# Performance work log

Measured on AMD Instinct MI355X. Metric: run time of the kernel, lower is better.

The kernel has to match this reference:

```python
import jax, jax.numpy as jnp
import numpy as np

B, N, IN_DIM, LATENT = 4, 4096, 1024, 128


def setup_inputs() -> dict:
    key = jax.random.key(0)
    ks = jax.random.split(key, 9)
    s_in = 1.0 / np.sqrt(IN_DIM)
    s_lat = 1.0 / np.sqrt(LATENT)
    return {
        "Q": jax.random.normal(ks[0], (B, N, IN_DIM), jnp.float32),
        "K": jax.random.normal(ks[1], (B, N, IN_DIM), jnp.float32),
        "V": jax.random.normal(ks[2], (B, N, IN_DIM), jnp.float32),
        "Wk": jax.random.uniform(ks[3], (LATENT, IN_DIM), jnp.float32, -s_in, s_in),
        "bk": jax.random.uniform(ks[4], (LATENT,), jnp.float32, -s_in, s_in),
        "Wq": jax.random.uniform(ks[5], (LATENT, LATENT), jnp.float32, -s_lat, s_lat),
        "bq": jax.random.uniform(ks[6], (LATENT,), jnp.float32, -s_lat, s_lat),
        "Wv": jax.random.uniform(ks[7], (LATENT, IN_DIM), jnp.float32, -s_in, s_in),
        "bv": jax.random.uniform(ks[8], (LATENT,), jnp.float32, -s_in, s_in),
    }


def reference(Q, K, V, Wk, bk, Wq, bq, Wv, bv):
    # NOTE: faithful to original quirks: input K is ignored; Q is re-projected
    # from key_prj(Q); qry_prj has in_dim == latent_dim for this to typecheck.
    Kp = jnp.einsum('bni,oi->bno', Q, Wk) + bk            # [B,N,LATENT]
    Qp = jnp.einsum('bnl,ol->bno', Kp, Wq) + bq           # [B,N,LATENT]
    Vp = jnp.einsum('bni,oi->bno', V, Wv) + bv            # [B,N,LATENT]
    n = Kp.shape[1]
    # score = bmm(K, Q^T) / sqrt(seq_len)  -> [B, N, N]
    scores = jnp.einsum('bnd,bmd->bnm', Kp, Qp) / jnp.sqrt(jnp.asarray(n, scores_dtype(Kp)))
    W = jax.nn.softmax(scores, axis=-2)                   # softmax over rows (dim=-2)
    # Y = (V^T @ W)^T = W^T @ V -> [B, N, LATENT]
    Y = jnp.einsum('bnm,bnd->bmd', W, Vp)
    return Y


def scores_dtype(x):
    return x.dtype
```

## Files before the change

kernel.cpp:

```cpp
#include <hip/hip_runtime.h>
#include <hip/hip_bf16.h>
#include <math.h>

#define NB     4
#define NTOK   4096
#define IND    1024
#define LAT    128
#define MTOT   (NB*NTOK)
#define L2E    1.4426950408889634f
#define SC2    0.022542110013890053f

typedef short bf16x8 __attribute__((ext_vector_type(8)));
typedef float f32x4  __attribute__((ext_vector_type(4)));
typedef float f32x16 __attribute__((ext_vector_type(16)));

__device__ __forceinline__ unsigned short f2bf(float x) {
    union { float f; unsigned int u; } v; v.f = x;
    unsigned int r = v.u + 0x7FFFu + ((v.u >> 16) & 1u);
    return (unsigned short)(r >> 16);
}
__device__ __forceinline__ float bf2f(unsigned short b) {
    union { unsigned int u; float f; } v; v.u = ((unsigned int)b) << 16;
    return v.f;
}
__device__ __forceinline__ unsigned cvtpk(float lo, float hi) {
    unsigned r;
    asm("v_cvt_pk_bf16_f32 %0, %1, %2" : "=v"(r) : "v"(lo), "v"(hi));
    return r;
}
__device__ __forceinline__ void permswap(unsigned &x, unsigned &y) {
    asm volatile("v_permlane32_swap_b32 %0, %1" : "+v"(x), "+v"(y));
}
__device__ __forceinline__ void gld16(const void* g, void* l) {
    __builtin_amdgcn_global_load_lds(
        (const __attribute__((address_space(1))) void*)g,
        (__attribute__((address_space(3))) void*)l, 16, 0, 0);
}

__global__ __launch_bounds__(256) void fuse_w(const float* __restrict__ Wq,
                                              const float* __restrict__ Wk,
                                              const float* __restrict__ bk,
                                              const float* __restrict__ bq,
                                              unsigned short* __restrict__ Wcomb,
                                              float* __restrict__ bqk) {
    const int o = blockIdx.y;
    const int i = blockIdx.x * 256 + threadIdx.x;
    Wcomb[(size_t)o * IND + i] = f2bf(Wk[(size_t)o * IND + i]);
    float acc = 0.f;
    #pragma unroll 8
    for (int l = 0; l < 128; ++l)
        acc = fmaf(Wq[o * 128 + l], Wk[(size_t)l * IND + i], acc);
    Wcomb[(size_t)(128 + o) * IND + i] = f2bf(acc * SC2);
    if (blockIdx.x == 0 && threadIdx.x == 0) {
        float b = bq[o];
        for (int l = 0; l < 128; ++l) b = fmaf(Wq[o * 128 + l], bk[l], b);
        bqk[o] = b * SC2;
    }
}

__global__ __launch_bounds__(256, 2) void proj_qk(const float* __restrict__ X,
                                                  const unsigned short* __restrict__ Wcomb,
                                                  const float* __restrict__ bk,
                                                  const float* __restrict__ bqk,
                                                  unsigned short* __restrict__ Kp,
                                                  unsigned short* __restrict__ Qp) {
    __shared__ __align__(16) char lds[4096 + 32768];
    const int t = threadIdx.x, l = t & 63, w = t >> 6;
    const int br = blockIdx.x;
    const int lrow = l & 15, lhi = l >> 4;
    const int wr = (w >> 1) * 16, wc = (w & 1) * 128;

    f32x4 acc[8] = {};

    float4 aR[2];
    bf16x8 bR[8];
    #pragma unroll
    for (int j = 0; j < 2; ++j) {
        int c = t + j * 256, row = c >> 4, ch = c & 15;
        aR[j] = *(const float4*)&X[(size_t)(br * 32 + row) * IND + ch * 4];
    }
    #pragma unroll
    for (int j = 0; j < 8; ++j) {
        int c = t + j * 256, row = c >> 3, ch = c & 7;
        bR[j] = *(const bf16x8*)&Wcomb[(size_t)row * IND + ch * 8];
    }

    for (int k0 = 0; k0 < IND; k0 += 64) {
        #pragma unroll
        for (int j = 0; j < 2; ++j) {
            int c = t + j * 256, row = c >> 4, ch = c & 15;
            union { unsigned short s[4]; unsigned long long q; } pk;
            pk.s[0] = f2bf(aR[j].x); pk.s[1] = f2bf(aR[j].y);
            pk.s[2] = f2bf(aR[j].z); pk.s[3] = f2bf(aR[j].w);
            *(unsigned long long*)(lds + ((row * 128 + ch * 8) ^ ((row & 7) << 4))) = pk.q;
        }
        #pragma unroll
        for (int j = 0; j < 8; ++j) {
            int c = t + j * 256, row = c >> 3, ch = c & 7;
            *(bf16x8*)(lds + 4096 + ((row * 128 + ch * 16) ^ ((row & 7) << 4))) = bR[j];
        }
        if (k0 + 64 < IND) {
            #pragma unroll
            for (int j = 0; j < 2; ++j) {
                int c = t + j * 256, row = c >> 4, ch = c & 15;
                aR[j] = *(const float4*)&X[(size_t)(br * 32 + row) * IND + k0 + 64 + ch * 4];
            }
            #pragma unroll
            for (int j = 0; j < 8; ++j) {
                int c = t + j * 256, row = c >> 3, ch = c & 7;
                bR[j] = *(const bf16x8*)&Wcomb[(size_t)row * IND + k0 + 64 + ch * 8];
            }
        }
        __syncthreads();

        const int arow = wr + lrow;
        bf16x8 a[2];
        #pragma unroll
        for (int kk = 0; kk < 2; ++kk)
            a[kk] = *(const bf16x8*)(lds + ((arow * 128 + kk * 64 + lhi * 16) ^ ((arow & 7) << 4)));
        #pragma unroll
        for (int n = 0; n < 8; ++n) {
            const int brow = wc + n * 16 + lrow;
            #pragma unroll
            for (int kk = 0; kk < 2; ++kk) {
                bf16x8 b = *(const bf16x8*)(lds + 4096 +
                    ((brow * 128 + kk * 64 + lhi * 16) ^ ((brow & 7) << 4)));
                acc[n] = __builtin_amdgcn_mfma_f32_16x16x32_bf16(a[kk], b, acc[n], 0, 0, 0);
            }
        }
        __syncthreads();
    }

    const int row0 = br * 32 + wr + lhi * 4;
    unsigned short* out = (wc == 0) ? Kp : Qp;
    const float* bias = (wc == 0) ? bk : bqk;
    #pragma unroll
    for (int n = 0; n < 8; ++n) {
        int col = n * 16 + lrow;
        float bv = bias[col];
        #pragma unroll
        for (int r = 0; r < 4; ++r)
            out[(size_t)(row0 + r) * LAT + col] = f2bf(acc[n][r] + bv);
    }
}

__global__ __launch_bounds__(256, 2) void proj_v(const float* __restrict__ X,
                                                 const float* __restrict__ Wv,
                                                 const float* __restrict__ bv,
                                                 unsigned short* __restrict__ VpT) {
    __shared__ __align__(16) char lds[4096 + 16384];
    const int t = threadIdx.x, l = t & 63, w = t >> 6;
    const int br = blockIdx.x;
    const int lrow = l & 15, lhi = l >> 4;
    const int wr = (w >> 1) * 16, wc = (w & 1) * 64;

    f32x4 acc[4] = {};

    float4 aR[2], bR[8];
    #pragma unroll
    for (int j = 0; j < 2; ++j) {
        int c = t + j * 256, row = c >> 4, ch = c & 15;
        aR[j] = *(const float4*)&X[(size_t)(br * 32 + row) * IND + ch * 4];
    }
    #pragma unroll
    for (int j = 0; j < 8; ++j) {
        int c = t + j * 256, row = c >> 4, ch = c & 15;
        bR[j] = *(const float4*)&Wv[(size_t)row * IND + ch * 4];
    }

    for (int k0 = 0; k0 < IND; k0 += 64) {
        #pragma unroll
        for (int j = 0; j < 2; ++j) {
            int c = t + j * 256, row = c >> 4, ch = c & 15;
            union { unsigned short s[4]; unsigned long long q; } pk;
            pk.s[0] = f2bf(aR[j].x); pk.s[1] = f2bf(aR[j].y);
            pk.s[2] = f2bf(aR[j].z); pk.s[3] = f2bf(aR[j].w);
            *(unsigned long long*)(lds + ((row * 128 + ch * 8) ^ ((row & 7) << 4))) = pk.q;
        }
        #pragma unroll
        for (int j = 0; j < 8; ++j) {
            int c = t + j * 256, row = c >> 4, ch = c & 15;
            union { unsigned short s[4]; unsigned long long q; } pk;
            pk.s[0] = f2bf(bR[j].x); pk.s[1] = f2bf(bR[j].y);
            pk.s[2] = f2bf(bR[j].z); pk.s[3] = f2bf(bR[j].w);
            *(unsigned long long*)(lds + 4096 + ((row * 128 + ch * 8) ^ ((row & 7) << 4))) = pk.q;
        }
        if (k0 + 64 < IND) {
            #pragma unroll
            for (int j = 0; j < 2; ++j) {
                int c = t + j * 256, row = c >> 4, ch = c & 15;
                aR[j] = *(const float4*)&X[(size_t)(br * 32 + row) * IND + k0 + 64 + ch * 4];
            }
            #pragma unroll
            for (int j = 0; j < 8; ++j) {
                int c = t + j * 256, row = c >> 4, ch = c & 15;
                bR[j] = *(const float4*)&Wv[(size_t)row * IND + k0 + 64 + ch * 4];
            }
        }
        __syncthreads();

        const int arow = wr + lrow;
        bf16x8 a[2];
        #pragma unroll
        for (int kk = 0; kk < 2; ++kk)
            a[kk] = *(const bf16x8*)(lds + ((arow * 128 + kk * 64 + lhi * 16) ^ ((arow & 7) << 4)));
        #pragma unroll
        for (int n = 0; n < 4; ++n) {
            const int brow = wc + n * 16 + lrow;
            #pragma unroll
            for (int kk = 0; kk < 2; ++kk) {
                bf16x8 b = *(const bf16x8*)(lds + 4096 +
                    ((brow * 128 + kk * 64 + lhi * 16) ^ ((brow & 7) << 4)));
                acc[n] = __builtin_amdgcn_mfma_f32_16x16x32_bf16(a[kk], b, acc[n], 0, 0, 0);
            }
        }
        __syncthreads();
    }

    const int row0 = br * 32 + wr + lhi * 4;
    const int batch = row0 >> 12, tok = row0 & 4095;
    #pragma unroll
    for (int n = 0; n < 4; ++n) {
        int col = wc + n * 16 + lrow;
        float bv_ = bv[col];
        union { unsigned short s[4]; unsigned long long q; } pk;
        #pragma unroll
        for (int r = 0; r < 4; ++r) pk.s[r] = f2bf(acc[n][r] + bv_);
        *(unsigned long long*)&VpT[(size_t)batch * (LAT * NTOK) + (size_t)col * NTOK + tok] = pk.q;
    }
}

template<int NSPLIT>
__global__ __launch_bounds__(256, 3) void attn4(const unsigned short* __restrict__ Qp,
                                                const unsigned short* __restrict__ Kp,
                                                const unsigned short* __restrict__ VpT,
                                                unsigned short* __restrict__ Opart,
                                                float* __restrict__ lsum,
                                                float* __restrict__ Y) {
    __shared__ __align__(16) char ldsK[2][8192];
    __shared__ __align__(16) char ldsV[2][8192];
    const int t = threadIdx.x, l = t & 63, w = t >> 6;
    const int lane31 = l & 31, hi = l >> 5;

    int qt, b, ck;
    if constexpr (NSPLIT > 1) {
        int x = blockIdx.x;
        int glo = x & 7, rest = x >> 3;
        qt = rest & 31;
        int g = glo + 8 * (rest >> 5);
        b = g / NSPLIT; ck = g % NSPLIT;
    } else {
        qt = blockIdx.x & 31; b = blockIdx.x >> 5; ck = 0;
    }
    const size_t base  = (size_t)b * ((size_t)NTOK * LAT);
    const size_t vbase = (size_t)b * ((size_t)LAT * NTOK);
    const int wq = qt * 128 + w * 32;
    const int k_base = ck * (NTOK / NSPLIT);
    const int kts = (NTOK / NSPLIT) / 32;

    const int kc_row = t >> 4, kc_ch = t & 15;
    const int vc_row = t >> 2, vc_ch = t & 3;

    bf16x8 qf[8];
    {
        const size_t qrow = base + (size_t)(wq + lane31) * LAT;
        #pragma unroll
        for (int ds = 0; ds < 8; ++ds)
            qf[ds] = *(const bf16x8*)&Qp[qrow + ds * 16 + hi * 8];
    }

    f32x16 OA[4] = {};
    float lrun = 0.f;

    auto STAGE = [&](int bi, int k_lo) {
        #pragma unroll
        for (int j = 0; j < 2; ++j) {
            int row = kc_row + j * 16;
            gld16(&Kp[base + (size_t)(k_lo + row) * LAT + (kc_ch ^ (row & 15)) * 8],
                  &ldsK[bi][j * 4096 + w * 1024]);
        }
        #pragma unroll
        for (int j = 0; j < 2; ++j) {
            int row = vc_row + j * 64;
            gld16(&VpT[vbase + (size_t)row * NTOK + k_lo + (vc_ch ^ ((row >> 1) & 3)) * 8],
                  &ldsV[bi][j * 4096 + w * 1024]);
        }
    };

    int buf = 0;
    STAGE(0, k_base);
    asm volatile("s_waitcnt vmcnt(0)" ::: "memory");
    __syncthreads();

    for (int kt = 0; kt < kts; ++kt) {
        if (kt + 1 < kts) STAGE(buf ^ 1, k_base + (kt + 1) * 32);
        const char* lK = ldsK[buf];
        const char* lV = ldsV[buf];

        f32x16 SA;
        {
            f32x16 s = {};
            const int kr = lane31;
            __builtin_amdgcn_s_setprio(1);
            #pragma unroll
            for (int ds = 0; ds < 8; ++ds) {
                bf16x8 kf = *(const bf16x8*)(lK +
                    ((kr * 256 + ds * 32 + hi * 16) ^ ((kr & 15) << 4)));
                s = __builtin_amdgcn_mfma_f32_32x32x16_bf16(kf, qf[ds], s, 0, 0, 0);
            }
            __builtin_amdgcn_s_setprio(0);
            SA = s;
        }

        float p[16];
        #pragma unroll
        for (int r = 0; r < 16; ++r) {
            p[r] = exp2f(SA[r]);
            lrun += p[r];
        }
        unsigned a0 = cvtpk(p[0], p[1]),  a1 = cvtpk(p[2], p[3]);
        unsigned a2 = cvtpk(p[4], p[5]),  a3 = cvtpk(p[6], p[7]);
        permswap(a0, a2); permswap(a1, a3);
        unsigned b0 = cvtpk(p[8], p[9]),   b1 = cvtpk(p[10], p[11]);
        unsigned b2 = cvtpk(p[12], p[13]), b3 = cvtpk(p[14], p[15]);
        permswap(b0, b2); permswap(b1, b3);
        union { unsigned u[4]; bf16x8 v; } f0 = {{a0, a1, a2, a3}};
        union { unsigned u[4]; bf16x8 v; } f1 = {{b0, b1, b2, b3}};

        __builtin_amdgcn_s_setprio(1);
        #pragma unroll
        for (int db = 0; db < 4; ++db) {
            const int d = db * 32 + lane31;
            const int vsw = ((d >> 1) & 3) << 4;
            bf16x8 vfA = *(const bf16x8*)(lV + ((d * 64 + hi * 16) ^ vsw));
            OA[db] = __builtin_amdgcn_mfma_f32_32x32x16_bf16(vfA, f0.v, OA[db], 0, 0, 0);
            bf16x8 vfB = *(const bf16x8*)(lV + ((d * 64 + 32 + hi * 16) ^ vsw));
            OA[db] = __builtin_amdgcn_mfma_f32_32x32x16_bf16(vfB, f1.v, OA[db], 0, 0, 0);
        }
        __builtin_amdgcn_s_setprio(0);

        asm volatile("s_waitcnt vmcnt(0)" ::: "memory");
        __syncthreads();
        buf ^= 1;
    }

    const float ltot = lrun + __shfl_xor(lrun, 32);

    if constexpr (NSPLIT == 1) {
        const float inv = 1.0f / ltot;
        float* dst = &Y[base + (size_t)(wq + lane31) * LAT];
        #pragma unroll
        for (int db = 0; db < 4; ++db)
            #pragma unroll
            for (int g = 0; g < 4; ++g) {
                f32x4 v;
                #pragma unroll
                for (int j = 0; j < 4; ++j) v[j] = OA[db][4 * g + j] * inv;
                *(f32x4*)&dst[db * 32 + 8 * g + 4 * hi] = v;
            }
    } else {
        const size_t prow = (size_t)ck * MTOT + (size_t)b * NTOK + wq + lane31;
        unsigned short* dst = &Opart[prow * LAT];
        #pragma unroll
        for (int db = 0; db < 4; ++db)
            #pragma unroll
            for (int g = 0; g < 4; ++g) {
                union { unsigned short s[4]; unsigned long long q; } pk;
                #pragma unroll
                for (int j = 0; j < 4; ++j) pk.s[j] = f2bf(OA[db][4 * g + j]);
                *(unsigned long long*)&dst[db * 32 + 8 * g + 4 * hi] = pk.q;
            }
        if (l < 32) lsum[prow] = ltot;
    }
}

template<int S>
__global__ __launch_bounds__(256) void merge3(const unsigned short* __restrict__ Opart,
                                              const float* __restrict__ lsum,
                                              float* __restrict__ Y) {
    const int idx = blockIdx.x * 256 + threadIdx.x;
    const int row = idx >> 4, cc = (idx & 15) * 8;
    float L = 0.f;
    #pragma unroll
    for (int c = 0; c < S; ++c) L += lsum[(size_t)c * MTOT + row];
    float acc[8] = {};
    #pragma unroll
    for (int c = 0; c < S; ++c) {
        bf16x8 v = *(const bf16x8*)&Opart[((size_t)c * MTOT + row) * LAT + cc];
        #pragma unroll
        for (int j = 0; j < 8; ++j)
            acc[j] += bf2f((unsigned short)v[j]);
    }
    const float inv = 1.f / L;
    f32x4 o0, o1;
    #pragma unroll
    for (int j = 0; j < 4; ++j) { o0[j] = acc[j] * inv; o1[j] = acc[4 + j] * inv; }
    *(f32x4*)&Y[(size_t)row * LAT + cc] = o0;
    *(f32x4*)&Y[(size_t)row * LAT + cc + 4] = o1;
}

extern "C" void kernel_launch(void* const* d_in, const int* in_sizes, int n_in,
                              void* d_out, int out_size, void* d_ws, size_t ws_size,
                              hipStream_t stream) {
    const float* Q  = (const float*)d_in[0];
    const float* V  = (const float*)d_in[2];
    const float* Wk = (const float*)d_in[3];
    const float* bk = (const float*)d_in[4];
    const float* Wq = (const float*)d_in[5];
    const float* bq = (const float*)d_in[6];
    const float* Wv = (const float*)d_in[7];
    const float* bv = (const float*)d_in[8];
    float* Y = (float*)d_out;

    char* ws = (char*)d_ws;
    unsigned short* Kp    = (unsigned short*)(ws);
    unsigned short* Qp    = (unsigned short*)(ws + (4 << 20));
    unsigned short* VpT   = (unsigned short*)(ws + (8 << 20));
    unsigned short* Wcomb = (unsigned short*)(ws + (12 << 20));
    float*          bqk   = (float*)         (ws + 13107200);
    float*          lsum  = (float*)         (ws + 13107712);
    unsigned short* Opart = (unsigned short*)(ws + 14680064);
    const size_t need8 = 14680064 + (size_t)8 * MTOT * LAT * 2;
    const size_t need4 = 14680064 + (size_t)4 * MTOT * LAT * 2;

    fuse_w<<<dim3(4, 128), 256, 0, stream>>>(Wq, Wk, bk, bq, Wcomb, bqk);
    proj_qk<<<dim3(512), 256, 0, stream>>>(Q, Wcomb, bk, bqk, Kp, Qp);
    proj_v<<<dim3(512), 256, 0, stream>>>(V, Wv, bv, VpT);

    if (ws_size >= need8) {
        attn4<8><<<dim3(32 * NB * 8), 256, 0, stream>>>(Qp, Kp, VpT, Opart, lsum, nullptr);
        merge3<8><<<dim3(MTOT * 16 / 256), 256, 0, stream>>>(Opart, lsum, Y);
    } else if (ws_size >= need4) {
        attn4<4><<<dim3(32 * NB * 4), 256, 0, stream>>>(Qp, Kp, VpT, Opart, lsum, nullptr);
        merge3<4><<<dim3(MTOT * 16 / 256), 256, 0, stream>>>(Opart, lsum, Y);
    } else {
        attn4<1><<<dim3(32 * NB), 256, 0, stream>>>(Qp, Kp, VpT, nullptr, nullptr, Y);
    }
}
```

Measured before the change: 116.2 us.

## Process two 32-query tiles per wave to reuse K/V LDS fragments

Each wave now handles 64 query rows (two 32-row sub-tiles) instead of 32. Every K and V fragment loaded from LDS feeds two MFMAs, which halves LDS reads and global K/V staging per query. Block count is halved and launch bounds drop to 2 blocks per CU, since register use roughly doubles with two sets of Q fragments and accumulators. The risks are lower occupancy and fewer blocks to fill the GPU (512 with NSPLIT=8).

```diff
diff --git a/kernel.cpp b/kernel.cpp
--- a/kernel.cpp
+++ b/kernel.cpp
@@ -231,7 +231,7 @@
 }
 
 template<int NSPLIT>
-__global__ __launch_bounds__(256, 3) void attn4(const unsigned short* __restrict__ Qp,
+__global__ __launch_bounds__(256, 2) void attn6(const unsigned short* __restrict__ Qp,
                                                 const unsigned short* __restrict__ Kp,
                                                 const unsigned short* __restrict__ VpT,
                                                 unsigned short* __restrict__ Opart,
@@ -246,31 +246,20 @@
     if constexpr (NSPLIT > 1) {
         int x = blockIdx.x;
         int glo = x & 7, rest = x >> 3;
-        qt = rest & 31;
-        int g = glo + 8 * (rest >> 5);
+        qt = rest & 15;
+        int g = glo + 8 * (rest >> 4);
         b = g / NSPLIT; ck = g % NSPLIT;
     } else {
-        qt = blockIdx.x & 31; b = blockIdx.x >> 5; ck = 0;
+        qt = blockIdx.x & 15; b = blockIdx.x >> 4; ck = 0;
     }
     const size_t base  = (size_t)b * ((size_t)NTOK * LAT);
     const size_t vbase = (size_t)b * ((size_t)LAT * NTOK);
-    const int wq = qt * 128 + w * 32;
+    const int wq = qt * 256 + w * 64;
     const int k_base = ck * (NTOK / NSPLIT);
     const int kts = (NTOK / NSPLIT) / 32;
 
     const int kc_row = t >> 4, kc_ch = t & 15;
     const int vc_row = t >> 2, vc_ch = t & 3;
-
-    bf16x8 qf[8];
-    {
-        const size_t qrow = base + (size_t)(wq + lane31) * LAT;
-        #pragma unroll
-        for (int ds = 0; ds < 8; ++ds)
-            qf[ds] = *(const bf16x8*)&Qp[qrow + ds * 16 + hi * 8];
-    }
-
-    f32x16 OA[4] = {};
-    float lrun = 0.f;
 
     auto STAGE = [&](int bi, int k_lo) {
         #pragma unroll
@@ -287,6 +276,20 @@
         }
     };
 
+    bf16x8 qf0[8], qf1[8];
+    {
+        const size_t qr0 = base + (size_t)(wq + lane31) * LAT;
+        const size_t qr1 = base + (size_t)(wq + 32 + lane31) * LAT;
+        #pragma unroll
+        for (int ds = 0; ds < 8; ++ds) {
+            qf0[ds] = *(const bf16x8*)&Qp[qr0 + ds * 16 + hi * 8];
+            qf1[ds] = *(const bf16x8*)&Qp[qr1 + ds * 16 + hi * 8];
+        }
+    }
+
+    f32x16 OA0[4] = {}, OA1[4] = {};
+    float lr0 = 0.f, lr1 = 0.f;
+
     int buf = 0;
     STAGE(0, k_base);
     asm volatile("s_waitcnt vmcnt(0)" ::: "memory");
@@ -297,35 +300,47 @@
         const char* lK = ldsK[buf];
         const char* lV = ldsV[buf];
 
-        f32x16 SA;
+        f32x16 SA0 = {}, SA1 = {};
         {
-            f32x16 s = {};
             const int kr = lane31;
+            const int ksw = (kr & 15) << 4;
             __builtin_amdgcn_s_setprio(1);
             #pragma unroll
             for (int ds = 0; ds < 8; ++ds) {
-                bf16x8 kf = *(const bf16x8*)(lK +
-                    ((kr * 256 + ds * 32 + hi * 16) ^ ((kr & 15) << 4)));
-                s = __builtin_amdgcn_mfma_f32_32x32x16_bf16(kf, qf[ds], s, 0, 0, 0);
+                bf16x8 kf = *(const bf16x8*)(lK + ((kr * 256 + ds * 32 + hi * 16) ^ ksw));
+                SA0 = __builtin_amdgcn_mfma_f32_32x32x16_bf16(kf, qf0[ds], SA0, 0, 0, 0);
+                SA1 = __builtin_amdgcn_mfma_f32_32x32x16_bf16(kf, qf1[ds], SA1, 0, 0, 0);
             }
             __builtin_amdgcn_s_setprio(0);
-            SA = s;
-        }
-
-        float p[16];
-        #pragma unroll
-        for (int r = 0; r < 16; ++r) {
-            p[r] = exp2f(SA[r]);
-            lrun += p[r];
-        }
-        unsigned a0 = cvtpk(p[0], p[1]),  a1 = cvtpk(p[2], p[3]);
-        unsigned a2 = cvtpk(p[4], p[5]),  a3 = cvtpk(p[6], p[7]);
-        permswap(a0, a2); permswap(a1, a3);
-        unsigned b0 = cvtpk(p[8], p[9]),   b1 = cvtpk(p[10], p[11]);
-        unsigned b2 = cvtpk(p[12], p[13]), b3 = cvtpk(p[14], p[15]);
-        permswap(b0, b2); permswap(b1, b3);
-        union { unsigned u[4]; bf16x8 v; } f0 = {{a0, a1, a2, a3}};
-        union { unsigned u[4]; bf16x8 v; } f1 = {{b0, b1, b2, b3}};
+        }
+
+        union { unsigned u[4]; bf16x8 v; } f00, f01, f10, f11;
+        {
+            float p[16];
+            #pragma unroll
+            for (int r = 0; r < 16; ++r) { p[r] = exp2f(SA0[r]); lr0 += p[r]; }
+            unsigned a0 = cvtpk(p[0], p[1]),  a1 = cvtpk(p[2], p[3]);
+            unsigned a2 = cvtpk(p[4], p[5]),  a3 = cvtpk(p[6], p[7]);
+            permswap(a0, a2); permswap(a1, a3);
+            unsigned b0 = cvtpk(p[8], p[9]),   b1 = cvtpk(p[10], p[11]);
+            unsigned b2 = cvtpk(p[12], p[13]), b3 = cvtpk(p[14], p[15]);
+            permswap(b0, b2); permswap(b1, b3);
+            f00.u[0]=a0; f00.u[1]=a1; f00.u[2]=a2; f00.u[3]=a3;
+            f01.u[0]=b0; f01.u[1]=b1; f01.u[2]=b2; f01.u[3]=b3;
+        }
+        {
+            float p[16];
+            #pragma unroll
+            for (int r = 0; r < 16; ++r) { p[r] = exp2f(SA1[r]); lr1 += p[r]; }
+            unsigned a0 = cvtpk(p[0], p[1]),  a1 = cvtpk(p[2], p[3]);
+            unsigned a2 = cvtpk(p[4], p[5]),  a3 = cvtpk(p[6], p[7]);
+            permswap(a0, a2); permswap(a1, a3);
+            unsigned b0 = cvtpk(p[8], p[9]),   b1 = cvtpk(p[10], p[11]);
+            unsigned b2 = cvtpk(p[12], p[13]), b3 = cvtpk(p[14], p[15]);
+            permswap(b0, b2); permswap(b1, b3);
+            f10.u[0]=a0; f10.u[1]=a1; f10.u[2]=a2; f10.u[3]=a3;
+            f11.u[0]=b0; f11.u[1]=b1; f11.u[2]=b2; f11.u[3]=b3;
+        }
 
         __builtin_amdgcn_s_setprio(1);
         #pragma unroll
@@ -333,9 +348,11 @@
             const int d = db * 32 + lane31;
             const int vsw = ((d >> 1) & 3) << 4;
             bf16x8 vfA = *(const bf16x8*)(lV + ((d * 64 + hi * 16) ^ vsw));
-            OA[db] = __builtin_amdgcn_mfma_f32_32x32x16_bf16(vfA, f0.v, OA[db], 0, 0, 0);
+            OA0[db] = __builtin_amdgcn_mfma_f32_32x32x16_bf16(vfA, f00.v, OA0[db], 0, 0, 0);
+            OA1[db] = __builtin_amdgcn_mfma_f32_32x32x16_bf16(vfA, f10.v, OA1[db], 0, 0, 0);
             bf16x8 vfB = *(const bf16x8*)(lV + ((d * 64 + 32 + hi * 16) ^ vsw));
-            OA[db] = __builtin_amdgcn_mfma_f32_32x32x16_bf16(vfB, f1.v, OA[db], 0, 0, 0);
+            OA0[db] = __builtin_amdgcn_mfma_f32_32x32x16_bf16(vfB, f01.v, OA0[db], 0, 0, 0);
+            OA1[db] = __builtin_amdgcn_mfma_f32_32x32x16_bf16(vfB, f11.v, OA1[db], 0, 0, 0);
         }
         __builtin_amdgcn_s_setprio(0);
 
@@ -344,33 +361,45 @@
         buf ^= 1;
     }
 
-    const float ltot = lrun + __shfl_xor(lrun, 32);
+    const float lt0 = lr0 + __shfl_xor(lr0, 32);
+    const float lt1 = lr1 + __shfl_xor(lr1, 32);
 
     if constexpr (NSPLIT == 1) {
-        const float inv = 1.0f / ltot;
-        float* dst = &Y[base + (size_t)(wq + lane31) * LAT];
+        const float i0 = 1.0f / lt0, i1 = 1.0f / lt1;
+        float* d0 = &Y[base + (size_t)(wq + lane31) * LAT];
+        float* d1 = &Y[base + (size_t)(wq + 32 + lane31) * LAT];
         #pragma unroll
         for (int db = 0; db < 4; ++db)
             #pragma unroll
             for (int g = 0; g < 4; ++g) {
-                f32x4 v;
+                f32x4 v0, v1;
                 #pragma unroll
-                for (int j = 0; j < 4; ++j) v[j] = OA[db][4 * g + j] * inv;
-                *(f32x4*)&dst[db * 32 + 8 * g + 4 * hi] = v;
+                for (int j = 0; j < 4; ++j) {
+                    v0[j] = OA0[db][4 * g + j] * i0;
+                    v1[j] = OA1[db][4 * g + j] * i1;
+                }
+                *(f32x4*)&d0[db * 32 + 8 * g + 4 * hi] = v0;
+                *(f32x4*)&d1[db * 32 + 8 * g + 4 * hi] = v1;
             }
     } else {
-        const size_t prow = (size_t)ck * MTOT + (size_t)b * NTOK + wq + lane31;
-        unsigned short* dst = &Opart[prow * LAT];
+        const size_t pr0 = (size_t)ck * MTOT + (size_t)b * NTOK + wq + lane31;
+        const size_t pr1 = pr0 + 32;
+        unsigned short* d0 = &Opart[pr0 * LAT];
+        unsigned short* d1 = &Opart[pr1 * LAT];
         #pragma unroll
         for (int db = 0; db < 4; ++db)
             #pragma unroll
             for (int g = 0; g < 4; ++g) {
-                union { unsigned short s[4]; unsigned long long q; } pk;
+                union { unsigned short s[4]; unsigned long long q; } p0, p1;
                 #pragma unroll
-                for (int j = 0; j < 4; ++j) pk.s[j] = f2bf(OA[db][4 * g + j]);
-                *(unsigned long long*)&dst[db * 32 + 8 * g + 4 * hi] = pk.q;
-            }
-        if (l < 32) lsum[prow] = ltot;
+                for (int j = 0; j < 4; ++j) {
+                    p0.s[j] = f2bf(OA0[db][4 * g + j]);
+                    p1.s[j] = f2bf(OA1[db][4 * g + j]);
+                }
+                *(unsigned long long*)&d0[db * 32 + 8 * g + 4 * hi] = p0.q;
+                *(unsigned long long*)&d1[db * 32 + 8 * g + 4 * hi] = p1.q;
+            }
+        if (l < 32) { lsum[pr0] = lt0; lsum[pr1] = lt1; }
     }
 }
 
@@ -428,12 +457,12 @@
     proj_v<<<dim3(512), 256, 0, stream>>>(V, Wv, bv, VpT);
 
     if (ws_size >= need8) {
-        attn4<8><<<dim3(32 * NB * 8), 256, 0, stream>>>(Qp, Kp, VpT, Opart, lsum, nullptr);
+        attn6<8><<<dim3(16 * NB * 8), 256, 0, stream>>>(Qp, Kp, VpT, Opart, lsum, nullptr);
         merge3<8><<<dim3(MTOT * 16 / 256), 256, 0, stream>>>(Opart, lsum, Y);
     } else if (ws_size >= need4) {
-        attn4<4><<<dim3(32 * NB * 4), 256, 0, stream>>>(Qp, Kp, VpT, Opart, lsum, nullptr);
+        attn6<4><<<dim3(16 * NB * 4), 256, 0, stream>>>(Qp, Kp, VpT, Opart, lsum, nullptr);
         merge3<4><<<dim3(MTOT * 16 / 256), 256, 0, stream>>>(Opart, lsum, Y);
     } else {
-        attn4<1><<<dim3(32 * NB), 256, 0, stream>>>(Qp, Kp, VpT, nullptr, nullptr, Y);
-    }
-}
+        attn6<1><<<dim3(16 * NB), 256, 0, stream>>>(Qp, Kp, VpT, nullptr, nullptr, Y);
+    }
+}
```

After: 128.2 us. +10.3%, slower.

## Merge QK and V projections into one launch and double attention key tile

Applied to the files above, without the earlier changes.

The QK and V projection kernels become one launch of 1024 blocks that branch on block index, which removes a launch and lets both GEMMs share the GPU. The attention kernel now stages 64 keys per iteration instead of 32, with larger LDS buffers, new swizzles, and occupancy lowered from 3 to 2 blocks per CU. It also drops the 8-way key split and defaults to a 4-way split, so there are fewer partial outputs to merge but less parallelism per kernel.

```diff
diff --git a/kernel.cpp b/kernel.cpp
--- a/kernel.cpp
+++ b/kernel.cpp
@@ -58,187 +58,184 @@
     }
 }
 
-__global__ __launch_bounds__(256, 2) void proj_qk(const float* __restrict__ X,
-                                                  const unsigned short* __restrict__ Wcomb,
-                                                  const float* __restrict__ bk,
-                                                  const float* __restrict__ bqk,
-                                                  unsigned short* __restrict__ Kp,
-                                                  unsigned short* __restrict__ Qp) {
+__global__ __launch_bounds__(256, 2) void proj_all(const float* __restrict__ Q,
+                                                   const unsigned short* __restrict__ Wcomb,
+                                                   const float* __restrict__ bk,
+                                                   const float* __restrict__ bqk,
+                                                   unsigned short* __restrict__ Kp,
+                                                   unsigned short* __restrict__ Qp,
+                                                   const float* __restrict__ V,
+                                                   const float* __restrict__ Wv,
+                                                   const float* __restrict__ bv,
+                                                   unsigned short* __restrict__ VpT) {
     __shared__ __align__(16) char lds[4096 + 32768];
     const int t = threadIdx.x, l = t & 63, w = t >> 6;
-    const int br = blockIdx.x;
     const int lrow = l & 15, lhi = l >> 4;
-    const int wr = (w >> 1) * 16, wc = (w & 1) * 128;
-
-    f32x4 acc[8] = {};
-
-    float4 aR[2];
-    bf16x8 bR[8];
-    #pragma unroll
-    for (int j = 0; j < 2; ++j) {
-        int c = t + j * 256, row = c >> 4, ch = c & 15;
-        aR[j] = *(const float4*)&X[(size_t)(br * 32 + row) * IND + ch * 4];
-    }
-    #pragma unroll
-    for (int j = 0; j < 8; ++j) {
-        int c = t + j * 256, row = c >> 3, ch = c & 7;
-        bR[j] = *(const bf16x8*)&Wcomb[(size_t)row * IND + ch * 8];
-    }
-
-    for (int k0 = 0; k0 < IND; k0 += 64) {
+
+    if (blockIdx.x < 512) {
+        const int br = blockIdx.x;
+        const int wr = (w >> 1) * 16, wc = (w & 1) * 128;
+        f32x4 acc[8] = {};
+
+        float4 aR[2];
+        bf16x8 bR[8];
         #pragma unroll
         for (int j = 0; j < 2; ++j) {
             int c = t + j * 256, row = c >> 4, ch = c & 15;
-            union { unsigned short s[4]; unsigned long long q; } pk;
-            pk.s[0] = f2bf(aR[j].x); pk.s[1] = f2bf(aR[j].y);
-            pk.s[2] = f2bf(aR[j].z); pk.s[3] = f2bf(aR[j].w);
-            *(unsigned long long*)(lds + ((row * 128 + ch * 8) ^ ((row & 7) << 4))) = pk.q;
+            aR[j] = *(const float4*)&Q[(size_t)(br * 32 + row) * IND + ch * 4];
         }
         #pragma unroll
         for (int j = 0; j < 8; ++j) {
             int c = t + j * 256, row = c >> 3, ch = c & 7;
-            *(bf16x8*)(lds + 4096 + ((row * 128 + ch * 16) ^ ((row & 7) << 4))) = bR[j];
-        }
-        if (k0 + 64 < IND) {
+            bR[j] = *(const bf16x8*)&Wcomb[(size_t)row * IND + ch * 8];
+        }
+
+        for (int k0 = 0; k0 < IND; k0 += 64) {
             #pragma unroll
             for (int j = 0; j < 2; ++j) {
                 int c = t + j * 256, row = c >> 4, ch = c & 15;
-                aR[j] = *(const float4*)&X[(size_t)(br * 32 + row) * IND + k0 + 64 + ch * 4];
+                union { unsigned short s[4]; unsigned long long q; } pk;
+                pk.s[0] = f2bf(aR[j].x); pk.s[1] = f2bf(aR[j].y);
+                pk.s[2] = f2bf(aR[j].z); pk.s[3] = f2bf(aR[j].w);
+                *(unsigned long long*)(lds + ((row * 128 + ch * 8) ^ ((row & 7) << 4))) = pk.q;
             }
             #pragma unroll
             for (int j = 0; j < 8; ++j) {
                 int c = t + j * 256, row = c >> 3, ch = c & 7;
-                bR[j] = *(const bf16x8*)&Wcomb[(size_t)row * IND + k0 + 64 + ch * 8];
-            }
-        }
-        __syncthreads();
-
-        const int arow = wr + lrow;
-        bf16x8 a[2];
-        #pragma unroll
-        for (int kk = 0; kk < 2; ++kk)
-            a[kk] = *(const bf16x8*)(lds + ((arow * 128 + kk * 64 + lhi * 16) ^ ((arow & 7) << 4)));
+                *(bf16x8*)(lds + 4096 + ((row * 128 + ch * 16) ^ ((row & 7) << 4))) = bR[j];
+            }
+            if (k0 + 64 < IND) {
+                #pragma unroll
+                for (int j = 0; j < 2; ++j) {
+                    int c = t + j * 256, row = c >> 4, ch = c & 15;
+                    aR[j] = *(const float4*)&Q[(size_t)(br * 32 + row) * IND + k0 + 64 + ch * 4];
+                }
+                #pragma unroll
+                for (int j = 0; j < 8; ++j) {
+                    int c = t + j * 256, row = c >> 3, ch = c & 7;
+                    bR[j] = *(const bf16x8*)&Wcomb[(size_t)row * IND + k0 + 64 + ch * 8];
+                }
+            }
+            __syncthreads();
+
+            const int arow = wr + lrow;
+            bf16x8 a[2];
+            #pragma unroll
+            for (int kk = 0; kk < 2; ++kk)
+                a[kk] = *(const bf16x8*)(lds + ((arow * 128 + kk * 64 + lhi * 16) ^ ((arow & 7) << 4)));
+            #pragma unroll
+            for (int n = 0; n < 8; ++n) {
+                const int brow = wc + n * 16 + lrow;
+                #pragma unroll
+                for (int kk = 0; kk < 2; ++kk) {
+                    bf16x8 b = *(const bf16x8*)(lds + 4096 +
+                        ((brow * 128 + kk * 64 + lhi * 16) ^ ((brow & 7) << 4)));
+                    acc[n] = __builtin_amdgcn_mfma_f32_16x16x32_bf16(a[kk], b, acc[n], 0, 0, 0);
+                }
+            }
+            __syncthreads();
+        }
+
+        const int row0 = br * 32 + wr + lhi * 4;
+        unsigned short* out = (wc == 0) ? Kp : Qp;
+        const float* bias = (wc == 0) ? bk : bqk;
         #pragma unroll
         for (int n = 0; n < 8; ++n) {
-            const int brow = wc + n * 16 + lrow;
-            #pragma unroll
-            for (int kk = 0; kk < 2; ++kk) {
-                bf16x8 b = *(const bf16x8*)(lds + 4096 +
-                    ((brow * 128 + kk * 64 + lhi * 16) ^ ((brow & 7) << 4)));
-                acc[n] = __builtin_amdgcn_mfma_f32_16x16x32_bf16(a[kk], b, acc[n], 0, 0, 0);
-            }
-        }
-        __syncthreads();
-    }
-
-    const int row0 = br * 32 + wr + lhi * 4;
-    unsigned short* out = (wc == 0) ? Kp : Qp;
-    const float* bias = (wc == 0) ? bk : bqk;
-    #pragma unroll
-    for (int n = 0; n < 8; ++n) {
-        int col = n * 16 + lrow;
-        float bv = bias[col];
-        #pragma unroll
-        for (int r = 0; r < 4; ++r)
-            out[(size_t)(row0 + r) * LAT + col] = f2bf(acc[n][r] + bv);
-    }
-}
-
-__global__ __launch_bounds__(256, 2) void proj_v(const float* __restrict__ X,
-                                                 const float* __restrict__ Wv,
-                                                 const float* __restrict__ bv,
-                                                 unsigned short* __restrict__ VpT) {
-    __shared__ __align__(16) char lds[4096 + 16384];
-    const int t = threadIdx.x, l = t & 63, w = t >> 6;
-    const int br = blockIdx.x;
-    const int lrow = l & 15, lhi = l >> 4;
-    const int wr = (w >> 1) * 16, wc = (w & 1) * 64;
-
-    f32x4 acc[4] = {};
-
-    float4 aR[2], bR[8];
-    #pragma unroll
-    for (int j = 0; j < 2; ++j) {
-        int c = t + j * 256, row = c >> 4, ch = c & 15;
-        aR[j] = *(const float4*)&X[(size_t)(br * 32 + row) * IND + ch * 4];
-    }
-    #pragma unroll
-    for (int j = 0; j < 8; ++j) {
-        int c = t + j * 256, row = c >> 4, ch = c & 15;
-        bR[j] = *(const float4*)&Wv[(size_t)row * IND + ch * 4];
-    }
-
-    for (int k0 = 0; k0 < IND; k0 += 64) {
+            int col = n * 16 + lrow;
+            float bv_ = bias[col];
+            #pragma unroll
+            for (int r = 0; r < 4; ++r)
+                out[(size_t)(row0 + r) * LAT + col] = f2bf(acc[n][r] + bv_);
+        }
+    } else {
+        const int br = blockIdx.x - 512;
+        const int wr = (w >> 1) * 16, wc = (w & 1) * 64;
+        f32x4 acc[4] = {};
+
+        float4 aR[2], bR[8];
         #pragma unroll
         for (int j = 0; j < 2; ++j) {
             int c = t + j * 256, row = c >> 4, ch = c & 15;
-            union { unsigned short s[4]; unsigned long long q; } pk;
-            pk.s[0] = f2bf(aR[j].x); pk.s[1] = f2bf(aR[j].y);
-            pk.s[2] = f2bf(aR[j].z); pk.s[3] = f2bf(aR[j].w);
-            *(unsigned long long*)(lds + ((row * 128 + ch * 8) ^ ((row & 7) << 4))) = pk.q;
+            aR[j] = *(const float4*)&V[(size_t)(br * 32 + row) * IND + ch * 4];
         }
         #pragma unroll
         for (int j = 0; j < 8; ++j) {
             int c = t + j * 256, row = c >> 4, ch = c & 15;
-            union { unsigned short s[4]; unsigned long long q; } pk;
-            pk.s[0] = f2bf(bR[j].x); pk.s[1] = f2bf(bR[j].y);
-            pk.s[2] = f2bf(bR[j].z); pk.s[3] = f2bf(bR[j].w);
-            *(unsigned long long*)(lds + 4096 + ((row * 128 + ch * 8) ^ ((row & 7) << 4))) = pk.q;
-        }
-        if (k0 + 64 < IND) {
+            bR[j] = *(const float4*)&Wv[(size_t)row * IND + ch * 4];
+        }
+
+        for (int k0 = 0; k0 < IND; k0 += 64) {
             #pragma unroll
             for (int j = 0; j < 2; ++j) {
                 int c = t + j * 256, row = c >> 4, ch = c & 15;
-                aR[j] = *(const float4*)&X[(size_t)(br * 32 + row) * IND + k0 + 64 + ch * 4];
+                union { unsigned short s[4]; unsigned long long q; } pk;
+                pk.s[0] = f2bf(aR[j].x); pk.s[1] = f2bf(aR[j].y);
+                pk.s[2] = f2bf(aR[j].z); pk.s[3] = f2bf(aR[j].w);
+                *(unsigned long long*)(lds + ((row * 128 + ch * 8) ^ ((row & 7) << 4))) = pk.q;
             }
             #pragma unroll
             for (int j = 0; j < 8; ++j) {
                 int c = t + j * 256, row = c >> 4, ch = c & 15;
-                bR[j] = *(const float4*)&Wv[(size_t)row * IND + k0 + 64 + ch * 4];
-            }
-        }
-        __syncthreads();
-
-        const int arow = wr + lrow;
-        bf16x8 a[2];
-        #pragma unroll
-        for (int kk = 0; kk < 2; ++kk)
-            a[kk] = *(const bf16x8*)(lds + ((arow * 128 + kk * 64 + lhi * 16) ^ ((arow & 7) << 4)));
+                union { unsigned short s[4]; unsigned long long q; } pk;
+                pk.s[0] = f2bf(bR[j].x); pk.s[1] = f2bf(bR[j].y);
+                pk.s[2] = f2bf(bR[j].z); pk.s[3] = f2bf(bR[j].w);
+                *(unsigned long long*)(lds + 4096 + ((row * 128 + ch * 8) ^ ((row & 7) << 4))) = pk.q;
+            }
+            if (k0 + 64 < IND) {
+                #pragma unroll
+                for (int j = 0; j < 2; ++j) {
+                    int c = t + j * 256, row = c >> 4, ch = c & 15;
+                    aR[j] = *(const float4*)&V[(size_t)(br * 32 + row) * IND + k0 + 64 + ch * 4];
+                }
+                #pragma unroll
+                for (int j = 0; j < 8; ++j) {
+                    int c = t + j * 256, row = c >> 4, ch = c & 15;
+                    bR[j] = *(const float4*)&Wv[(size_t)row * IND + k0 + 64 + ch * 4];
+                }
+            }
+            __syncthreads();
+
+            const int arow = wr + lrow;
+            bf16x8 a[2];
+            #pragma unroll
+            for (int kk = 0; kk < 2; ++kk)
+                a[kk] = *(const bf16x8*)(lds + ((arow * 128 + kk * 64 + lhi * 16) ^ ((arow & 7) << 4)));
+            #pragma unroll
+            for (int n = 0; n < 4; ++n) {
+                const int brow = wc + n * 16 + lrow;
+                #pragma unroll
+                for (int kk = 0; kk < 2; ++kk) {
+                    bf16x8 b = *(const bf16x8*)(lds + 4096 +
+                        ((brow * 128 + kk * 64 + lhi * 16) ^ ((brow & 7) << 4)));
+                    acc[n] = __builtin_amdgcn_mfma_f32_16x16x32_bf16(a[kk], b, acc[n], 0, 0, 0);
+                }
+            }
+            __syncthreads();
+        }
+
+        const int row0 = br * 32 + wr + lhi * 4;
+        const int batch = row0 >> 12, tok = row0 & 4095;
         #pragma unroll
         for (int n = 0; n < 4; ++n) {
-            const int brow = wc + n * 16 + lrow;
-            #pragma unroll
-            for (int kk = 0; kk < 2; ++kk) {
-                bf16x8 b = *(const bf16x8*)(lds + 4096 +
-                    ((brow * 128 + kk * 64 + lhi * 16) ^ ((brow & 7) << 4)));
-                acc[n] = __builtin_amdgcn_mfma_f32_16x16x32_bf16(a[kk], b, acc[n], 0, 0, 0);
-            }
-        }
-        __syncthreads();
-    }
-
-    const int row0 = br * 32 + wr + lhi * 4;
-    const int batch = row0 >> 12, tok = row0 & 4095;
-    #pragma unroll
-    for (int n = 0; n < 4; ++n) {
-        int col = wc + n * 16 + lrow;
-        float bv_ = bv[col];
-        union { unsigned short s[4]; unsigned long long q; } pk;
-        #pragma unroll
-        for (int r = 0; r < 4; ++r) pk.s[r] = f2bf(acc[n][r] + bv_);
-        *(unsigned long long*)&VpT[(size_t)batch * (LAT * NTOK) + (size_t)col * NTOK + tok] = pk.q;
+            int col = wc + n * 16 + lrow;
+            float bv_ = bv[col];
+            union { unsigned short s[4]; unsigned long long q; } pk;
+            #pragma unroll
+            for (int r = 0; r < 4; ++r) pk.s[r] = f2bf(acc[n][r] + bv_);
+            *(unsigned long long*)&VpT[(size_t)batch * (LAT * NTOK) + (size_t)col * NTOK + tok] = pk.q;
+        }
     }
 }
 
 template<int NSPLIT>
-__global__ __launch_bounds__(256, 3) void attn4(const unsigned short* __restrict__ Qp,
+__global__ __launch_bounds__(256, 2) void attn7(const unsigned short* __restrict__ Qp,
                                                 const unsigned short* __restrict__ Kp,
                                                 const unsigned short* __restrict__ VpT,
                                                 unsigned short* __restrict__ Opart,
                                                 float* __restrict__ lsum,
                                                 float* __restrict__ Y) {
-    __shared__ __align__(16) char ldsK[2][8192];
-    __shared__ __align__(16) char ldsV[2][8192];
+    __shared__ __align__(16) char ldsK[2][16384];
+    __shared__ __align__(16) char ldsV[2][16384];
     const int t = threadIdx.x, l = t & 63, w = t >> 6;
     const int lane31 = l & 31, hi = l >> 5;
 
@@ -256,10 +253,25 @@
     const size_t vbase = (size_t)b * ((size_t)LAT * NTOK);
     const int wq = qt * 128 + w * 32;
     const int k_base = ck * (NTOK / NSPLIT);
-    const int kts = (NTOK / NSPLIT) / 32;
+    const int kts = (NTOK / NSPLIT) / 64;
 
     const int kc_row = t >> 4, kc_ch = t & 15;
-    const int vc_row = t >> 2, vc_ch = t & 3;
+    const int vc_row = t >> 3, vc_ch = t & 7;
+
+    auto STAGE = [&](int bi, int k_lo) {
+        #pragma unroll
+        for (int j = 0; j < 4; ++j) {
+            int row = kc_row + j * 16;
+            gld16(&Kp[base + (size_t)(k_lo + row) * LAT + (kc_ch ^ (row & 15)) * 8],
+                  &ldsK[bi][j * 4096 + w * 1024]);
+        }
+        #pragma unroll
+        for (int j = 0; j < 4; ++j) {
+            int row = vc_row + j * 32;
+            gld16(&VpT[vbase + (size_t)row * NTOK + k_lo + (vc_ch ^ (row & 7)) * 8],
+                  &ldsV[bi][j * 4096 + w * 1024]);
+        }
+    };
 
     bf16x8 qf[8];
     {
@@ -271,21 +283,6 @@
 
     f32x16 OA[4] = {};
     float lrun = 0.f;
-
-    auto STAGE = [&](int bi, int k_lo) {
-        #pragma unroll
-        for (int j = 0; j < 2; ++j) {
-            int row = kc_row + j * 16;
-            gld16(&Kp[base + (size_t)(k_lo + row) * LAT + (kc_ch ^ (row & 15)) * 8],
-                  &ldsK[bi][j * 4096 + w * 1024]);
-        }
-        #pragma unroll
-        for (int j = 0; j < 2; ++j) {
-            int row = vc_row + j * 64;
-            gld16(&VpT[vbase + (size_t)row * NTOK + k_lo + (vc_ch ^ ((row >> 1) & 3)) * 8],
-                  &ldsV[bi][j * 4096 + w * 1024]);
-        }
-    };
 
     int buf = 0;
     STAGE(0, k_base);
@@ -293,51 +290,55 @@
     __syncthreads();
 
     for (int kt = 0; kt < kts; ++kt) {
-        if (kt + 1 < kts) STAGE(buf ^ 1, k_base + (kt + 1) * 32);
+        if (kt + 1 < kts) STAGE(buf ^ 1, k_base + (kt + 1) * 64);
         const char* lK = ldsK[buf];
         const char* lV = ldsV[buf];
 
-        f32x16 SA;
-        {
+        f32x16 SA[2];
+        __builtin_amdgcn_s_setprio(1);
+        #pragma unroll
+        for (int kb = 0; kb < 2; ++kb) {
             f32x16 s = {};
-            const int kr = lane31;
+            const int kr = kb * 32 + lane31;
+            const int ksw = (kr & 15) << 4;
+            #pragma unroll
+            for (int ds = 0; ds < 8; ++ds) {
+                bf16x8 kf = *(const bf16x8*)(lK + ((kr * 256 + ds * 32 + hi * 16) ^ ksw));
+                s = __builtin_amdgcn_mfma_f32_32x32x16_bf16(kf, qf[ds], s, 0, 0, 0);
+            }
+            SA[kb] = s;
+        }
+        __builtin_amdgcn_s_setprio(0);
+
+        #pragma unroll
+        for (int kb = 0; kb < 2; ++kb) {
+            float p[16];
+            #pragma unroll
+            for (int r = 0; r < 16; ++r) {
+                p[r] = exp2f(SA[kb][r]);
+                lrun += p[r];
+            }
+            unsigned a0 = cvtpk(p[0], p[1]),  a1 = cvtpk(p[2], p[3]);
+            unsigned a2 = cvtpk(p[4], p[5]),  a3 = cvtpk(p[6], p[7]);
+            permswap(a0, a2); permswap(a1, a3);
+            unsigned b0 = cvtpk(p[8], p[9]),   b1 = cvtpk(p[10], p[11]);
+            unsigned b2 = cvtpk(p[12], p[13]), b3 = cvtpk(p[14], p[15]);
+            permswap(b0, b2); permswap(b1, b3);
+            union { unsigned u[4]; bf16x8 v; } f0 = {{a0, a1, a2, a3}};
+            union { unsigned u[4]; bf16x8 v; } f1 = {{b0, b1, b2, b3}};
+
             __builtin_amdgcn_s_setprio(1);
             #pragma unroll
-            for (int ds = 0; ds < 8; ++ds) {
-                bf16x8 kf = *(const bf16x8*)(lK +
-                    ((kr * 256 + ds * 32 + hi * 16) ^ ((kr & 15) << 4)));
-                s = __builtin_amdgcn_mfma_f32_32x32x16_bf16(kf, qf[ds], s, 0, 0, 0);
+            for (int db = 0; db < 4; ++db) {
+                const int d = db * 32 + lane31;
+                const int vsw = (d & 7) << 4;
+                bf16x8 vfA = *(const bf16x8*)(lV + ((d * 128 + (kb * 2 + 0) * 32 + hi * 16) ^ vsw));
+                OA[db] = __builtin_amdgcn_mfma_f32_32x32x16_bf16(vfA, f0.v, OA[db], 0, 0, 0);
+                bf16x8 vfB = *(const bf16x8*)(lV + ((d * 128 + (kb * 2 + 1) * 32 + hi * 16) ^ vsw));
+                OA[db] = __builtin_amdgcn_mfma_f32_32x32x16_bf16(vfB, f1.v, OA[db], 0, 0, 0);
             }
             __builtin_amdgcn_s_setprio(0);
-            SA = s;
-        }
-
-        float p[16];
-        #pragma unroll
-        for (int r = 0; r < 16; ++r) {
-            p[r] = exp2f(SA[r]);
-            lrun += p[r];
-        }
-        unsigned a0 = cvtpk(p[0], p[1]),  a1 = cvtpk(p[2], p[3]);
-        unsigned a2 = cvtpk(p[4], p[5]),  a3 = cvtpk(p[6], p[7]);
-        permswap(a0, a2); permswap(a1, a3);
-        unsigned b0 = cvtpk(p[8], p[9]),   b1 = cvtpk(p[10], p[11]);
-        unsigned b2 = cvtpk(p[12], p[13]), b3 = cvtpk(p[14], p[15]);
-        permswap(b0, b2); permswap(b1, b3);
-        union { unsigned u[4]; bf16x8 v; } f0 = {{a0, a1, a2, a3}};
-        union { unsigned u[4]; bf16x8 v; } f1 = {{b0, b1, b2, b3}};
-
-        __builtin_amdgcn_s_setprio(1);
-        #pragma unroll
-        for (int db = 0; db < 4; ++db) {
-            const int d = db * 32 + lane31;
-            const int vsw = ((d >> 1) & 3) << 4;
-            bf16x8 vfA = *(const bf16x8*)(lV + ((d * 64 + hi * 16) ^ vsw));
-            OA[db] = __builtin_amdgcn_mfma_f32_32x32x16_bf16(vfA, f0.v, OA[db], 0, 0, 0);
-            bf16x8 vfB = *(const bf16x8*)(lV + ((d * 64 + 32 + hi * 16) ^ vsw));
-            OA[db] = __builtin_amdgcn_mfma_f32_32x32x16_bf16(vfB, f1.v, OA[db], 0, 0, 0);
-        }
-        __builtin_amdgcn_s_setprio(0);
+        }
 
         asm volatile("s_waitcnt vmcnt(0)" ::: "memory");
         __syncthreads();
@@ -420,20 +421,15 @@
     float*          bqk   = (float*)         (ws + 13107200);
     float*          lsum  = (float*)         (ws + 13107712);
     unsigned short* Opart = (unsigned short*)(ws + 14680064);
-    const size_t need8 = 14680064 + (size_t)8 * MTOT * LAT * 2;
     const size_t need4 = 14680064 + (size_t)4 * MTOT * LAT * 2;
 
     fuse_w<<<dim3(4, 128), 256, 0, stream>>>(Wq, Wk, bk, bq, Wcomb, bqk);
-    proj_qk<<<dim3(512), 256, 0, stream>>>(Q, Wcomb, bk, bqk, Kp, Qp);
-    proj_v<<<dim3(512), 256, 0, stream>>>(V, Wv, bv, VpT);
-
-    if (ws_size >= need8) {
-        attn4<8><<<dim3(32 * NB * 8), 256, 0, stream>>>(Qp, Kp, VpT, Opart, lsum, nullptr);
-        merge3<8><<<dim3(MTOT * 16 / 256), 256, 0, stream>>>(Opart, lsum, Y);
-    } else if (ws_size >= need4) {
-        attn4<4><<<dim3(32 * NB * 4), 256, 0, stream>>>(Qp, Kp, VpT, Opart, lsum, nullptr);
+    proj_all<<<dim3(1024), 256, 0, stream>>>(Q, Wcomb, bk, bqk, Kp, Qp, V, Wv, bv, VpT);
+
+    if (ws_size >= need4) {
+        attn7<4><<<dim3(32 * NB * 4), 256, 0, stream>>>(Qp, Kp, VpT, Opart, lsum, nullptr);
         merge3<4><<<dim3(MTOT * 16 / 256), 256, 0, stream>>>(Opart, lsum, Y);
     } else {
-        attn4<1><<<dim3(32 * NB), 256, 0, stream>>>(Qp, Kp, VpT, nullptr, nullptr, Y);
-    }
-}
+        attn7<1><<<dim3(32 * NB), 256, 0, stream>>>(Qp, Kp, VpT, nullptr, nullptr, Y);
+    }
+}
```

Result: faster. 103.2 us (median of 3 runs) (-11.3%).
